# Kernel optimization log

Hardware: AMD Instinct MI355X
Metric: run time of the kernel (lower is better)

The kernel has to match this reference:

```python
import jax, jax.numpy as jnp
import numpy as np

NW = 8            # qubits per circuit
DIM = 2 ** NW     # 256 state-vector amplitudes
ATTN_WIRES = [0, 1, 2, 3, 4, 5, 6, 7]
FFN_WIRES = [0, 1, 2, 2, 4, 5, 6, 7]   # faithful bug: input 3 -> wire 2, wire 3 never encoded

# PauliZ sign of wire w for basis state idx (wire 0 = most significant bit, torchquantum layout)
_bits = (np.arange(DIM)[None, :] >> (NW - 1 - np.arange(NW)[:, None])) & 1
SIGNS = jnp.asarray(1.0 - 2.0 * _bits, dtype=jnp.float32)  # (8, 256)


def _rx(state, theta, w):
    """Apply RX(theta) on wire w. state: (N, 256) complex64, theta: (N,) float."""
    a, b = 2 ** w, 2 ** (NW - 1 - w)
    s = state.reshape(-1, a, 2, b)
    c = jnp.cos(theta * 0.5).astype(jnp.complex64)[:, None, None]
    sn = jnp.sin(theta * 0.5).astype(jnp.complex64)[:, None, None]
    s0, s1 = s[:, :, 0, :], s[:, :, 1, :]
    n0 = c * s0 - 1j * sn * s1
    n1 = -1j * sn * s0 + c * s1
    return jnp.stack([n0, n1], axis=2).reshape(-1, DIM)


def _cnot(state, c, t):
    """CNOT with control c, target t on (N, 256) state."""
    s = state.reshape((-1,) + (2,) * NW)
    s = jnp.moveaxis(s, (1 + c, 1 + t), (1, 2))
    s = jnp.concatenate([s[:, :1], s[:, 1:, ::-1]], axis=1)  # flip target where control==1
    s = jnp.moveaxis(s, (1, 2), (1 + c, 1 + t))
    return s.reshape(-1, DIM)


def qlayer(angles, thetas, wires):
    """Encoder RX(angles) per wire map, trainable RX, CNOT ring, PauliZ expectations.
    angles: (N, 8); thetas: (8,). Returns (N, 8) float32."""
    n = angles.shape[0]
    state = jnp.zeros((n, DIM), jnp.complex64).at[:, 0].set(1.0)  # |0...0>
    for i, w in enumerate(wires):
        state = _rx(state, angles[:, i], w)
    for w in range(NW):
        state = _rx(state, jnp.broadcast_to(thetas[w], (n,)), w)
    for k in range(NW):
        state = _cnot(state, k, (k + 1) % NW)
    probs = jnp.abs(state) ** 2          # (N, 256)
    return probs @ SIGNS.T               # (N, 8)


def layernorm(x, w, b, eps=1e-5):
    m = x.mean(-1, keepdims=True)
    v = x.var(-1, keepdims=True)
    return (x - m) / jnp.sqrt(v + eps) * w + b


def setup_inputs() -> dict:
    key = jax.random.key(0)
    ks = jax.random.split(key, 8)
    B, T, E = 128, 512, 8
    return {
        "x": jax.random.normal(ks[0], (B, T, E), jnp.float32),
        "thetas_attn": jax.random.normal(ks[1], (8,), jnp.float32),
        "thetas_ffn": jax.random.normal(ks[2], (8,), jnp.float32),
        "W_in": jax.random.normal(ks[3], (8, 8), jnp.float32) * (1.0 / np.sqrt(8)),
        "b_in": jax.random.normal(ks[4], (8,), jnp.float32) * 0.02,
        "W_out": jax.random.normal(ks[5], (8, 8), jnp.float32) * (1.0 / np.sqrt(8)),
        "b_out": jax.random.normal(ks[6], (8,), jnp.float32) * 0.02,
        "ln1_w": jnp.ones((8,), jnp.float32),
        "ln1_b": jnp.zeros((8,), jnp.float32),
        "ln2_w": jnp.ones((8,), jnp.float32),
        "ln2_b": jnp.zeros((8,), jnp.float32),
    }


def reference(x, thetas_attn, thetas_ffn, W_in, b_in, W_out, b_out,
              ln1_w, ln1_b, ln2_w, ln2_b):
    B, T, E = x.shape
    H = 2
    dk = E // H
    flat = x.reshape(B * T, E)
    # Q, K, V are the same quantum layer on the same input -> identical tensors
    qkv = qlayer(flat, thetas_attn, ATTN_WIRES).reshape(B, T, E)
    h = qkv.reshape(B, T, H, dk).transpose(0, 2, 1, 3)           # (B, H, T, dk)
    scores = jnp.einsum('bhqd,bhkd->bhqk', h, h) / jnp.sqrt(jnp.float32(dk))
    w_attn = jax.nn.softmax(scores, axis=-1)
    ctx = jnp.einsum('bhqk,bhkd->bhqd', w_attn, h)
    ctx = ctx.transpose(0, 2, 1, 3).reshape(B, T, E)
    # quantum output projection of the attention result
    attn_out = qlayer(ctx.reshape(B * T, E), thetas_attn, ATTN_WIRES).reshape(B, T, E)
    x1 = layernorm(attn_out + x, ln1_w, ln1_b)                   # dropout identity (eval)
    # quantum feed-forward: linear_in -> circuit (input detached in torch) -> linear_out
    hq = x1 @ W_in.T + b_in
    q = qlayer(jax.lax.stop_gradient(hq.reshape(B * T, E)), thetas_ffn, FFN_WIRES)
    ff = q.reshape(B, T, E) @ W_out.T + b_out
    return layernorm(ff + x1, ln2_w, ln2_b)
```

## Files before the change

### kernel.cpp

```cpp
#include <hip/hip_runtime.h>


__device__ __forceinline__ void zprod8(const float z[8], float out[8]) {
    float p = z[0];
#pragma unroll
    for (int w = 1; w < 8; ++w) { p *= z[w]; out[w] = p; }
    float q = z[1];
#pragma unroll
    for (int w = 2; w < 8; ++w) q *= z[w];
    out[0] = q;
}

__global__ __launch_bounds__(256) void k_attn(const float* __restrict__ x,
                                              const float* __restrict__ tha,
                                              float* __restrict__ ctx) {
    const int qt = blockIdx.x & 1;
    const int hh = (blockIdx.x >> 1) & 1;
    const int b  = blockIdx.x >> 2;
    const int tid = threadIdx.x;

    __shared__ float4 kvs[512];

    float th[8];
#pragma unroll
    for (int w = 0; w < 8; ++w) th[w] = tha[w];

#pragma unroll
    for (int rr = 0; rr < 2; ++rr) {
        const int r = tid + rr * 256;
        const float4* xp = (const float4*)(x + ((size_t)b * 512 + r) * 8);
        const float4 a = xp[0];
        const float4 bb = xp[1];
        const float ang[8] = {a.x, a.y, a.z, a.w, bb.x, bb.y, bb.z, bb.w};
        float z[8], o[8];
#pragma unroll
        for (int w = 0; w < 8; ++w) z[w] = cosf(ang[w] + th[w]);
        zprod8(z, o);
        kvs[r] = hh ? make_float4(o[4], o[5], o[6], o[7])
                    : make_float4(o[0], o[1], o[2], o[3]);
    }
    __syncthreads();

    const int qrow = qt * 256 + tid;
    float4 qv = kvs[qrow];
    qv.x *= 0.5f; qv.y *= 0.5f; qv.z *= 0.5f; qv.w *= 0.5f;

    float l = 0.0f;
    float4 acc = make_float4(0.f, 0.f, 0.f, 0.f);
#pragma unroll 8
    for (int k = 0; k < 512; ++k) {
        const float4 kk = kvs[k];
        const float s = qv.x * kk.x + qv.y * kk.y + qv.z * kk.z + qv.w * kk.w;
        const float p = __expf(s);
        l += p;
        acc.x += p * kk.x; acc.y += p * kk.y;
        acc.z += p * kk.z; acc.w += p * kk.w;
    }
    const float inv = 1.0f / l;
    float4 o = make_float4(acc.x * inv, acc.y * inv, acc.z * inv, acc.w * inv);
    *(float4*)(ctx + ((size_t)b * 512 + qrow) * 8 + hh * 4) = o;
}

__global__ __launch_bounds__(256) void k_tail(const float* __restrict__ x,
                                              float* io,
                                              const float* __restrict__ tha,
                                              const float* __restrict__ thf,
                                              const float* __restrict__ Win,
                                              const float* __restrict__ bin,
                                              const float* __restrict__ Wout,
                                              const float* __restrict__ bout,
                                              const float* __restrict__ ln1w,
                                              const float* __restrict__ ln1b,
                                              const float* __restrict__ ln2w,
                                              const float* __restrict__ ln2b) {
    const int t = blockIdx.x * 256 + threadIdx.x;

    const float4* xp = (const float4*)(x + (size_t)t * 8);
    const float4 xa = xp[0], xb = xp[1];
    const float xv[8] = {xa.x, xa.y, xa.z, xa.w, xb.x, xb.y, xb.z, xb.w};

    const float4* cp = (const float4*)(io + (size_t)t * 8);
    const float4 ca = cp[0], cb = cp[1];
    const float cv[8] = {ca.x, ca.y, ca.z, ca.w, cb.x, cb.y, cb.z, cb.w};

    float z[8], ao[8];
#pragma unroll
    for (int w = 0; w < 8; ++w) z[w] = cosf(cv[w] + tha[w]);
    zprod8(z, ao);

    float y[8];
    float m = 0.f;
#pragma unroll
    for (int i = 0; i < 8; ++i) { y[i] = ao[i] + xv[i]; m += y[i]; }
    m *= 0.125f;
    float v = 0.f;
#pragma unroll
    for (int i = 0; i < 8; ++i) { const float d = y[i] - m; v += d * d; }
    v *= 0.125f;
    float r = rsqrtf(v + 1e-5f);
    float x1[8];
#pragma unroll
    for (int i = 0; i < 8; ++i) x1[i] = (y[i] - m) * r * ln1w[i] + ln1b[i];

    float hq[8];
#pragma unroll
    for (int i = 0; i < 8; ++i) {
        float s = bin[i];
#pragma unroll
        for (int j = 0; j < 8; ++j) s += x1[j] * Win[i * 8 + j];
        hq[i] = s;
    }

    float phi[8];
    phi[0] = hq[0] + thf[0];
    phi[1] = hq[1] + thf[1];
    phi[2] = hq[2] + hq[3] + thf[2];
    phi[3] = thf[3];
    phi[4] = hq[4] + thf[4];
    phi[5] = hq[5] + thf[5];
    phi[6] = hq[6] + thf[6];
    phi[7] = hq[7] + thf[7];
    float qq[8];
#pragma unroll
    for (int w = 0; w < 8; ++w) z[w] = cosf(phi[w]);
    zprod8(z, qq);

    float y2[8];
    float m2 = 0.f;
#pragma unroll
    for (int i = 0; i < 8; ++i) {
        float s = bout[i];
#pragma unroll
        for (int j = 0; j < 8; ++j) s += qq[j] * Wout[i * 8 + j];
        y2[i] = s + x1[i];
        m2 += y2[i];
    }
    m2 *= 0.125f;
    float v2 = 0.f;
#pragma unroll
    for (int i = 0; i < 8; ++i) { const float d = y2[i] - m2; v2 += d * d; }
    v2 *= 0.125f;
    const float r2 = rsqrtf(v2 + 1e-5f);

    float o[8];
#pragma unroll
    for (int i = 0; i < 8; ++i) o[i] = (y2[i] - m2) * r2 * ln2w[i] + ln2b[i];

    float4* op = (float4*)(io + (size_t)t * 8);
    op[0] = make_float4(o[0], o[1], o[2], o[3]);
    op[1] = make_float4(o[4], o[5], o[6], o[7]);
}

extern "C" void kernel_launch(void* const* d_in, const int* in_sizes, int n_in,
                              void* d_out, int out_size, void* d_ws, size_t ws_size,
                              hipStream_t stream) {
    const float* x    = (const float*)d_in[0];
    const float* tha  = (const float*)d_in[1];
    const float* thf  = (const float*)d_in[2];
    const float* Win  = (const float*)d_in[3];
    const float* bin  = (const float*)d_in[4];
    const float* Wout = (const float*)d_in[5];
    const float* bout = (const float*)d_in[6];
    const float* ln1w = (const float*)d_in[7];
    const float* ln1b = (const float*)d_in[8];
    const float* ln2w = (const float*)d_in[9];
    const float* ln2b = (const float*)d_in[10];
    float* out = (float*)d_out;

    k_attn<<<512, 256, 0, stream>>>(x, tha, out);
    k_tail<<<256, 256, 0, stream>>>(x, out, tha, thf, Win, bin, Wout, bout,
                                    ln1w, ln1b, ln2w, ln2b);
}
```

Measured before the change: 107.3 us.

## Fuse attention and tail into one kernel with both heads per block

Merges the attention kernel and the post-attention tail into a single launch. Each 512-thread block now handles both heads for half the queries, so the quantum K/V encoding of a sequence is computed once per block rather than once per head. The context vector is exchanged through shared memory instead of a round trip through global memory. Also switches to fast __cosf, exp2f with the log2(e) factor folded into the query, and explicit FMAs. In exchange, half the threads sit idle during the tail, the launch has half as many blocks, and the fast intrinsics lose some accuracy.

```diff
diff --git a/kernel.cpp b/kernel.cpp
--- a/kernel.cpp
+++ b/kernel.cpp
@@ -11,144 +11,143 @@
     out[0] = q;
 }
 
-__global__ __launch_bounds__(256) void k_attn(const float* __restrict__ x,
-                                              const float* __restrict__ tha,
-                                              float* __restrict__ ctx) {
-    const int qt = blockIdx.x & 1;
-    const int hh = (blockIdx.x >> 1) & 1;
-    const int b  = blockIdx.x >> 2;
-    const int tid = threadIdx.x;
+__global__ __launch_bounds__(512) void k_fused(const float* __restrict__ x,
+                                               const float* __restrict__ tha,
+                                               const float* __restrict__ thf,
+                                               const float* __restrict__ Win,
+                                               const float* __restrict__ bin,
+                                               const float* __restrict__ Wout,
+                                               const float* __restrict__ bout,
+                                               const float* __restrict__ ln1w,
+                                               const float* __restrict__ ln1b,
+                                               const float* __restrict__ ln2w,
+                                               const float* __restrict__ ln2b,
+                                               float* __restrict__ out) {
+    const int qhalf = blockIdx.x & 1;
+    const int b     = blockIdx.x >> 1;
+    const int tid   = threadIdx.x;
+    const int h     = tid >> 8;
+    const int r     = tid & 255;
 
-    __shared__ float4 kvs[512];
+    __shared__ float4 kvs[512][2];
 
-    float th[8];
-#pragma unroll
-    for (int w = 0; w < 8; ++w) th[w] = tha[w];
-
-#pragma unroll
-    for (int rr = 0; rr < 2; ++rr) {
-        const int r = tid + rr * 256;
-        const float4* xp = (const float4*)(x + ((size_t)b * 512 + r) * 8);
-        const float4 a = xp[0];
+    {
+        const float4* xp = (const float4*)(x + ((size_t)b * 512 + tid) * 8);
+        const float4 a  = xp[0];
         const float4 bb = xp[1];
         const float ang[8] = {a.x, a.y, a.z, a.w, bb.x, bb.y, bb.z, bb.w};
         float z[8], o[8];
 #pragma unroll
-        for (int w = 0; w < 8; ++w) z[w] = cosf(ang[w] + th[w]);
+        for (int w = 0; w < 8; ++w) z[w] = __cosf(ang[w] + tha[w]);
         zprod8(z, o);
-        kvs[r] = hh ? make_float4(o[4], o[5], o[6], o[7])
-                    : make_float4(o[0], o[1], o[2], o[3]);
+        kvs[tid][0] = make_float4(o[0], o[1], o[2], o[3]);
+        kvs[tid][1] = make_float4(o[4], o[5], o[6], o[7]);
     }
     __syncthreads();
 
-    const int qrow = qt * 256 + tid;
-    float4 qv = kvs[qrow];
-    qv.x *= 0.5f; qv.y *= 0.5f; qv.z *= 0.5f; qv.w *= 0.5f;
+    const int qrow = qhalf * 256 + r;
+    float4 qv = kvs[qrow][h];
+    const float sc = 0.5f * 1.44269504088896f;
+    qv.x *= sc; qv.y *= sc; qv.z *= sc; qv.w *= sc;
 
-    float l = 0.0f;
+    float  l   = 0.0f;
     float4 acc = make_float4(0.f, 0.f, 0.f, 0.f);
 #pragma unroll 8
     for (int k = 0; k < 512; ++k) {
-        const float4 kk = kvs[k];
-        const float s = qv.x * kk.x + qv.y * kk.y + qv.z * kk.z + qv.w * kk.w;
-        const float p = __expf(s);
+        const float4 kk = kvs[k][h];
+        const float s = fmaf(qv.x, kk.x,
+                        fmaf(qv.y, kk.y,
+                        fmaf(qv.z, kk.z, qv.w * kk.w)));
+        const float p = exp2f(s);
         l += p;
-        acc.x += p * kk.x; acc.y += p * kk.y;
-        acc.z += p * kk.z; acc.w += p * kk.w;
+        acc.x = fmaf(p, kk.x, acc.x);
+        acc.y = fmaf(p, kk.y, acc.y);
+        acc.z = fmaf(p, kk.z, acc.z);
+        acc.w = fmaf(p, kk.w, acc.w);
     }
     const float inv = 1.0f / l;
-    float4 o = make_float4(acc.x * inv, acc.y * inv, acc.z * inv, acc.w * inv);
-    *(float4*)(ctx + ((size_t)b * 512 + qrow) * 8 + hh * 4) = o;
-}
+    const float4 cvh = make_float4(acc.x * inv, acc.y * inv,
+                                   acc.z * inv, acc.w * inv);
 
-__global__ __launch_bounds__(256) void k_tail(const float* __restrict__ x,
-                                              float* io,
-                                              const float* __restrict__ tha,
-                                              const float* __restrict__ thf,
-                                              const float* __restrict__ Win,
-                                              const float* __restrict__ bin,
-                                              const float* __restrict__ Wout,
-                                              const float* __restrict__ bout,
-                                              const float* __restrict__ ln1w,
-                                              const float* __restrict__ ln1b,
-                                              const float* __restrict__ ln2w,
-                                              const float* __restrict__ ln2b) {
-    const int t = blockIdx.x * 256 + threadIdx.x;
+    __syncthreads();
+    kvs[r][h] = cvh;
+    __syncthreads();
 
-    const float4* xp = (const float4*)(x + (size_t)t * 8);
-    const float4 xa = xp[0], xb = xp[1];
-    const float xv[8] = {xa.x, xa.y, xa.z, xa.w, xb.x, xb.y, xb.z, xb.w};
+    if (tid < 256) {
+        const size_t t = (size_t)b * 512 + qhalf * 256 + tid;
 
-    const float4* cp = (const float4*)(io + (size_t)t * 8);
-    const float4 ca = cp[0], cb = cp[1];
-    const float cv[8] = {ca.x, ca.y, ca.z, ca.w, cb.x, cb.y, cb.z, cb.w};
+        const float4 ca = kvs[tid][0], cb = kvs[tid][1];
+        const float cv[8] = {ca.x, ca.y, ca.z, ca.w, cb.x, cb.y, cb.z, cb.w};
 
-    float z[8], ao[8];
+        const float4* xp = (const float4*)(x + t * 8);
+        const float4 xa = xp[0], xb = xp[1];
+        const float xv[8] = {xa.x, xa.y, xa.z, xa.w, xb.x, xb.y, xb.z, xb.w};
+
+        float z[8], ao[8];
 #pragma unroll
-    for (int w = 0; w < 8; ++w) z[w] = cosf(cv[w] + tha[w]);
-    zprod8(z, ao);
+        for (int w = 0; w < 8; ++w) z[w] = __cosf(cv[w] + tha[w]);
+        zprod8(z, ao);
 
-    float y[8];
-    float m = 0.f;
+        float y[8], m = 0.f;
 #pragma unroll
-    for (int i = 0; i < 8; ++i) { y[i] = ao[i] + xv[i]; m += y[i]; }
-    m *= 0.125f;
-    float v = 0.f;
+        for (int i = 0; i < 8; ++i) { y[i] = ao[i] + xv[i]; m += y[i]; }
+        m *= 0.125f;
+        float v = 0.f;
 #pragma unroll
-    for (int i = 0; i < 8; ++i) { const float d = y[i] - m; v += d * d; }
-    v *= 0.125f;
-    float r = rsqrtf(v + 1e-5f);
-    float x1[8];
+        for (int i = 0; i < 8; ++i) { const float d = y[i] - m; v += d * d; }
+        v *= 0.125f;
+        const float rs = rsqrtf(v + 1e-5f);
+        float x1[8];
 #pragma unroll
-    for (int i = 0; i < 8; ++i) x1[i] = (y[i] - m) * r * ln1w[i] + ln1b[i];
+        for (int i = 0; i < 8; ++i) x1[i] = (y[i] - m) * rs * ln1w[i] + ln1b[i];
 
-    float hq[8];
+        float hq[8];
 #pragma unroll
-    for (int i = 0; i < 8; ++i) {
-        float s = bin[i];
+        for (int i = 0; i < 8; ++i) {
+            float s = bin[i];
 #pragma unroll
-        for (int j = 0; j < 8; ++j) s += x1[j] * Win[i * 8 + j];
-        hq[i] = s;
+            for (int j = 0; j < 8; ++j) s = fmaf(x1[j], Win[i * 8 + j], s);
+            hq[i] = s;
+        }
+
+        float phi[8];
+        phi[0] = hq[0] + thf[0];
+        phi[1] = hq[1] + thf[1];
+        phi[2] = hq[2] + hq[3] + thf[2];
+        phi[3] = thf[3];
+        phi[4] = hq[4] + thf[4];
+        phi[5] = hq[5] + thf[5];
+        phi[6] = hq[6] + thf[6];
+        phi[7] = hq[7] + thf[7];
+        float qq[8];
+#pragma unroll
+        for (int w = 0; w < 8; ++w) z[w] = __cosf(phi[w]);
+        zprod8(z, qq);
+
+        float y2[8], m2 = 0.f;
+#pragma unroll
+        for (int i = 0; i < 8; ++i) {
+            float s = bout[i];
+#pragma unroll
+            for (int j = 0; j < 8; ++j) s = fmaf(qq[j], Wout[i * 8 + j], s);
+            y2[i] = s + x1[i];
+            m2 += y2[i];
+        }
+        m2 *= 0.125f;
+        float v2 = 0.f;
+#pragma unroll
+        for (int i = 0; i < 8; ++i) { const float d = y2[i] - m2; v2 += d * d; }
+        v2 *= 0.125f;
+        const float r2 = rsqrtf(v2 + 1e-5f);
+
+        float o[8];
+#pragma unroll
+        for (int i = 0; i < 8; ++i) o[i] = (y2[i] - m2) * r2 * ln2w[i] + ln2b[i];
+
+        float4* op = (float4*)(out + t * 8);
+        op[0] = make_float4(o[0], o[1], o[2], o[3]);
+        op[1] = make_float4(o[4], o[5], o[6], o[7]);
     }
-
-    float phi[8];
-    phi[0] = hq[0] + thf[0];
-    phi[1] = hq[1] + thf[1];
-    phi[2] = hq[2] + hq[3] + thf[2];
-    phi[3] = thf[3];
-    phi[4] = hq[4] + thf[4];
-    phi[5] = hq[5] + thf[5];
-    phi[6] = hq[6] + thf[6];
-    phi[7] = hq[7] + thf[7];
-    float qq[8];
-#pragma unroll
-    for (int w = 0; w < 8; ++w) z[w] = cosf(phi[w]);
-    zprod8(z, qq);
-
-    float y2[8];
-    float m2 = 0.f;
-#pragma unroll
-    for (int i = 0; i < 8; ++i) {
-        float s = bout[i];
-#pragma unroll
-        for (int j = 0; j < 8; ++j) s += qq[j] * Wout[i * 8 + j];
-        y2[i] = s + x1[i];
-        m2 += y2[i];
-    }
-    m2 *= 0.125f;
-    float v2 = 0.f;
-#pragma unroll
-    for (int i = 0; i < 8; ++i) { const float d = y2[i] - m2; v2 += d * d; }
-    v2 *= 0.125f;
-    const float r2 = rsqrtf(v2 + 1e-5f);
-
-    float o[8];
-#pragma unroll
-    for (int i = 0; i < 8; ++i) o[i] = (y2[i] - m2) * r2 * ln2w[i] + ln2b[i];
-
-    float4* op = (float4*)(io + (size_t)t * 8);
-    op[0] = make_float4(o[0], o[1], o[2], o[3]);
-    op[1] = make_float4(o[4], o[5], o[6], o[7]);
 }
 
 extern "C" void kernel_launch(void* const* d_in, const int* in_sizes, int n_in,
@@ -167,7 +166,6 @@
     const float* ln2b = (const float*)d_in[10];
     float* out = (float*)d_out;
 
-    k_attn<<<512, 256, 0, stream>>>(x, tha, out);
-    k_tail<<<256, 256, 0, stream>>>(x, out, tha, thf, Win, bin, Wout, bout,
-                                    ln1w, ln1b, ln2w, ln2b);
+    k_fused<<<256, 512, 0, stream>>>(x, tha, thf, Win, bin, Wout, bout,
+                                     ln1w, ln1b, ln2w, ln2b, out);
 }
```

New measurement: 101.8 us. 5.1% less time.
